# Performance work log

Measured on AMD Instinct MI355X. Metric: run time of the kernel, lower is better.

## Reference

```python
import jax, jax.numpy as jnp
import numpy as np

B, T, D, NH = 4, 2048, 768, 12
DH = D // NH
NEG = -100000.0  # module uses masked_fill with -100000.0, not -inf


def setup_inputs() -> dict:
    key = jax.random.key(0)
    ks = jax.random.split(key, 9)
    s = 1.0 / np.sqrt(D)
    return {
        "x": jax.random.normal(ks[0], (B, T, D), jnp.float32),
        "wq": jax.random.normal(ks[1], (D, D), jnp.float32) * s,
        "bq": jax.random.normal(ks[2], (D,), jnp.float32) * 0.02,
        "wk": jax.random.normal(ks[3], (D, D), jnp.float32) * s,
        "bk": jax.random.normal(ks[4], (D,), jnp.float32) * 0.02,
        "wv": jax.random.normal(ks[5], (D, D), jnp.float32) * s,
        "bv": jax.random.normal(ks[6], (D,), jnp.float32) * 0.02,
        "wo": jax.random.normal(ks[7], (D, D), jnp.float32) * s,
        "bo": jax.random.normal(ks[8], (D,), jnp.float32) * 0.02,
    }


def reference(x, wq, bq, wk, bk, wv, bv, wo, bo):
    Bx, Tx, E = x.shape
    # torch Linear: y = x @ W.T + b, weight shape [out, in]
    def heads(w, b):
        return (x @ w.T + b).reshape(Bx, Tx, NH, DH).transpose(0, 2, 1, 3)  # [B,nh,T,dh]
    Q, K, V = heads(wq, bq), heads(wk, bk), heads(wv, bv)
    scale = 1.0 / jnp.sqrt(jnp.float32(DH))
    QK = jnp.einsum("bhqd,bhkd->bhqk", Q, K) * scale  # [B,nh,T,T]
    causal = jnp.tril(jnp.ones((Tx, Tx), dtype=bool))
    QK = jnp.where(causal, QK, NEG)
    A = jax.nn.softmax(QK, axis=-1)  # attn_dropout p=0 (eval)
    Z = jnp.einsum("bhqk,bhkd->bhqd", A, V)
    Z = Z.transpose(0, 2, 1, 3).reshape(Bx, Tx, E)
    return Z @ wo.T + bo  # resid_dropout p=0 (eval)
```

## Files before the change

kernel.cpp:

```cpp
#include <hip/hip_runtime.h>


#define B_ 4
#define T_ 2048
#define D_ 768
#define NH_ 12
#define DH_ 64
#define M_ (B_ * T_)

typedef __attribute__((ext_vector_type(8))) short bf16x8;
typedef __attribute__((ext_vector_type(4))) float f32x4;
typedef __attribute__((ext_vector_type(16))) float f32x16;
typedef __attribute__((ext_vector_type(4))) unsigned int u32x4;

__device__ __forceinline__ unsigned short f2bf(float f) {
  unsigned int u = __builtin_bit_cast(unsigned int, f);
  u += 0x7FFFu + ((u >> 16) & 1u);
  return (unsigned short)(u >> 16);
}

__device__ __forceinline__ void async16(const void* g, void* l) {
  __builtin_amdgcn_global_load_lds(
      (const __attribute__((address_space(1))) unsigned int*)g,
      (__attribute__((address_space(3))) unsigned int*)l, 16, 0, 0);
}

#define RAW_BARRIER()                         \
  do {                                        \
    asm volatile("" ::: "memory");            \
    __builtin_amdgcn_s_barrier();             \
    asm volatile("" ::: "memory");            \
  } while (0)

__global__ void cvt_kernel(const float* __restrict__ x, const float* __restrict__ wq,
                           const float* __restrict__ wk, const float* __restrict__ wv,
                           const float* __restrict__ wo,
                           unsigned short* __restrict__ xb, unsigned short* __restrict__ wqb,
                           unsigned short* __restrict__ wkb, unsigned short* __restrict__ wvb,
                           unsigned short* __restrict__ wob) {
  const float* src; unsigned short* dst; int n4;
  switch (blockIdx.y) {
    case 0: src = x;  dst = xb;  n4 = M_ * D_ / 4; break;
    case 1: src = wq; dst = wqb; n4 = D_ * D_ / 4; break;
    case 2: src = wk; dst = wkb; n4 = D_ * D_ / 4; break;
    case 3: src = wv; dst = wvb; n4 = D_ * D_ / 4; break;
    default: src = wo; dst = wob; n4 = D_ * D_ / 4; break;
  }
  int stride = gridDim.x * blockDim.x;
  for (int i = blockIdx.x * blockDim.x + threadIdx.x; i < n4; i += stride) {
    float4 v = ((const float4*)src)[i];
    ushort4 o;
    o.x = f2bf(v.x); o.y = f2bf(v.y); o.z = f2bf(v.z); o.w = f2bf(v.w);
    ((ushort4*)dst)[i] = o;
  }
}

__global__ __launch_bounds__(512, 4) void gemm_kernel(
    const unsigned short* __restrict__ A,
    const unsigned short* __restrict__ W0, const unsigned short* __restrict__ W1,
    const unsigned short* __restrict__ W2,
    const float* __restrict__ bias0, const float* __restrict__ bias1,
    const float* __restrict__ bias2,
    void* out0, void* out1, void* out2,
    float s0, int K, int qkv) {
  __shared__ __align__(16) char lds[73728];

  int bid = blockIdx.x;
  int xcd = bid & 7, g = bid >> 3;
  int mt, nt;
  if (qkv) { mt = xcd + (g / 9) * 8; nt = g % 9; }
  else     { mt = xcd + (g / 3) * 8;  nt = g % 3; }
  int y  = qkv ? nt / 3 : 0;
  int nW = qkv ? nt % 3 : nt;
  const unsigned short* W = y == 0 ? W0 : (y == 1 ? W1 : W2);
  const float* bias = y == 0 ? bias0 : (y == 1 ? bias1 : bias2);
  void* outp = y == 0 ? out0 : (y == 1 ? out1 : out2);
  float scl = (qkv && y == 0) ? s0 : 1.0f;
  int mode = qkv ? ((y == 2) ? 2 : 1) : 0;

  int tid = threadIdx.x, lane = tid & 63, wid = tid >> 6;
  int l15 = lane & 15, l4 = lane >> 4;
  int wm = wid >> 2, wn = wid & 3;
  int m0 = mt << 7, n0w = nW << 8;

  int aRow, aCol;
  {
    int row = wid * 16 + (lane >> 2);
    int colE = (lane & 3) * 8;
    aRow = row;
    aCol = colE ^ (((row >> 1) & 3) << 3);
  }
  int bRow[2], bCol[2];
#pragma unroll
  for (int c = 0; c < 2; ++c) {
    int u = c * 8 + wid;
    int row = u * 16 + (lane >> 2);
    int colE = (lane & 3) * 8;
    bRow[c] = row;
    bCol[c] = colE ^ (((row >> 1) & 3) << 3);
  }

  int aoff[4], boff[4];
#pragma unroll
  for (int mf = 0; mf < 4; ++mf) {
    int row = wm * 64 + mf * 16 + l15;
    aoff[mf] = row * 64 + ((l4 * 16) ^ (((row >> 1) & 3) << 4));
  }
#pragma unroll
  for (int nf = 0; nf < 4; ++nf) {
    int row = wn * 64 + nf * 16 + l15;
    boff[nf] = 8192 + row * 64 + ((l4 * 16) ^ (((row >> 1) & 3) << 4));
  }

  const unsigned short* Wb = W + (size_t)n0w * K;

#define ISSUE_TILE(kt, slot)                                                       \
  do {                                                                             \
    async16(A + (size_t)(m0 + aRow) * K + (kt) + aCol, (slot) + wid * 1024);       \
    _Pragma("unroll") for (int c = 0; c < 2; ++c)                                  \
      async16(Wb + (size_t)bRow[c] * K + (kt) + bCol[c],                           \
              (slot) + 8192 + (c * 8 + wid) * 1024);                               \
  } while (0)

  f32x4 acc[4][4] = {};
  char* b0 = lds;
  char* b1 = lds + 24576;
  char* b2 = lds + 49152;

  ISSUE_TILE(0, b0);
  ISSUE_TILE(32, b1);

  int NT = K >> 5;
#pragma unroll 1
  for (int t = 0; t < NT; ++t) {
    if (t + 1 < NT) asm volatile("s_waitcnt vmcnt(3)" ::: "memory");
    else            asm volatile("s_waitcnt vmcnt(0)" ::: "memory");
    RAW_BARRIER();
    if (t + 2 < NT) ISSUE_TILE((t + 2) << 5, b2);
    bf16x8 af[4], bfr[4];
#pragma unroll
    for (int mf = 0; mf < 4; ++mf) af[mf] = *(const bf16x8*)(b0 + aoff[mf]);
#pragma unroll
    for (int nf = 0; nf < 4; ++nf) bfr[nf] = *(const bf16x8*)(b0 + boff[nf]);
    __builtin_amdgcn_s_setprio(1);
#pragma unroll
    for (int mf = 0; mf < 4; ++mf)
#pragma unroll
      for (int nf = 0; nf < 4; ++nf)
        acc[mf][nf] = __builtin_amdgcn_mfma_f32_16x16x32_bf16(af[mf], bfr[nf], acc[mf][nf], 0, 0, 0);
    __builtin_amdgcn_s_setprio(0);
    char* tmp = b0; b0 = b1; b1 = b2; b2 = tmp;
  }
#undef ISSUE_TILE

  if (mode == 2) {
#pragma unroll
    for (int nf = 0; nf < 4; ++nf) {
      int colW = n0w + wn * 64 + nf * 16 + l15;
      float bv = bias[colW];
      int h = colW >> 6, d = colW & 63;
#pragma unroll
      for (int mf = 0; mf < 4; ++mf) {
        int rbase = m0 + wm * 64 + mf * 16 + l4 * 4;
        int bb = rbase >> 11, tt = rbase & (T_ - 1);
        ushort4 o;
        o.x = f2bf(acc[mf][nf][0] + bv);
        o.y = f2bf(acc[mf][nf][1] + bv);
        o.z = f2bf(acc[mf][nf][2] + bv);
        o.w = f2bf(acc[mf][nf][3] + bv);
        *(ushort4*)((unsigned short*)outp + ((size_t)(bb * NH_ + h) * DH_ + d) * T_ + tt) = o;
      }
    }
  } else {
#pragma unroll
    for (int nf = 0; nf < 4; ++nf) {
      int colW = n0w + wn * 64 + nf * 16 + l15;
      float bv = bias[colW];
#pragma unroll
      for (int mf = 0; mf < 4; ++mf) {
        int rbase = m0 + wm * 64 + mf * 16 + l4 * 4;
#pragma unroll
        for (int r = 0; r < 4; ++r) {
          float v = (acc[mf][nf][r] + bv) * scl;
          size_t idx = (size_t)(rbase + r) * D_ + colW;
          if (mode == 1) ((unsigned short*)outp)[idx] = f2bf(v);
          else           ((float*)outp)[idx] = v;
        }
      }
    }
  }
}

__global__ __launch_bounds__(256, 2) void attn_kernel(
    const unsigned short* __restrict__ Q, const unsigned short* __restrict__ Kg,
    const unsigned short* __restrict__ VT, unsigned short* __restrict__ Z) {
  __shared__ __align__(16) char lds[65536];

  int tid = threadIdx.x, lane = tid & 63, w = tid >> 6;
  int l31 = lane & 31, hi = lane >> 5;
  int bid = blockIdx.x;
  int xcd = bid & 7, g = bid >> 3;
  int qt = 15 - g / 6;
  int bh = xcd + (g % 6) * 8;
  int b = bh / NH_, h = bh % NH_;
  int q0 = qt * 128;
  int qrow = q0 + w * 32 + l31;

  const unsigned short* Qb = Q + (size_t)(b * T_) * D_ + h * DH_;
  const unsigned short* Kb = Kg + (size_t)(b * T_) * D_ + h * DH_;
  const unsigned short* VTb = VT + (size_t)(b * NH_ + h) * DH_ * T_;

  bf16x8 qf[4];
#pragma unroll
  for (int s = 0; s < 4; ++s)
    qf[s] = *(const bf16x8*)(Qb + (size_t)qrow * D_ + s * 16 + hi * 8);

  int sRow[2], sCol[2];
#pragma unroll
  for (int c = 0; c < 2; ++c) {
    int pos = ((c * 4 + w) * 64 + lane) * 8;
    int row = pos >> 6, colE = pos & 63;
    sRow[c] = row;
    sCol[c] = colE ^ ((row & 7) << 3);
  }

  int koff[2][4];
#pragma unroll
  for (int n = 0; n < 2; ++n)
#pragma unroll
    for (int s = 0; s < 4; ++s) {
      int row = n * 32 + l31;
      koff[n][s] = row * 128 + ((s * 32 + hi * 16) ^ ((row & 7) << 4));
    }

  f32x16 zt[2] = {};
  float l_run = 0.f;
  int ntiles = 2 * qt + 2;

#define STAGE(tt)                                                                  \
  do {                                                                             \
    int kv0 = (tt) * 64;                                                           \
    int kb = ((tt) & 3) << 13;                                                     \
    _Pragma("unroll") for (int c = 0; c < 2; ++c) {                                \
      async16(Kb + (size_t)(kv0 + sRow[c]) * D_ + sCol[c],                         \
              lds + kb + (c * 4 + w) * 1024);                                      \
      async16(VTb + (size_t)sRow[c] * T_ + kv0 + sCol[c],                          \
              lds + 32768 + kb + (c * 4 + w) * 1024);                              \
    }                                                                              \
  } while (0)

  STAGE(0);
  STAGE(1);

#pragma unroll 1
  for (int t = 0; t < ntiles; ++t) {
    if ((t & 1) == 0) {
      __syncthreads();
      if (t + 2 < ntiles) {
        STAGE(t + 2);
        STAGE(t + 3);
      }
    }
    const char* kbase = lds + ((t & 3) << 13);
    const char* vbase = lds + 32768 + ((t & 3) << 13);

    f32x16 st[2];
    __builtin_amdgcn_s_setprio(1);
#pragma unroll
    for (int n = 0; n < 2; ++n) {
      f32x16 a = {};
#pragma unroll
      for (int s = 0; s < 4; ++s) {
        bf16x8 kf = *(const bf16x8*)(kbase + koff[n][s]);
        a = __builtin_amdgcn_mfma_f32_32x32x16_bf16(kf, qf[s], a, 0, 0, 0);
      }
      st[n] = a;
    }
    __builtin_amdgcn_s_setprio(0);

    if (t >= 2 * qt) {
      int kvb = t * 64;
#pragma unroll
      for (int n = 0; n < 2; ++n)
#pragma unroll
        for (int m = 0; m < 4; ++m)
#pragma unroll
          for (int c2 = 0; c2 < 4; ++c2) {
            int kv = kvb + n * 32 + m * 8 + hi * 4 + c2;
            if (kv > qrow) st[n][m * 4 + c2] = -1e30f;
          }
    }

    bf16x8 pb[4];
#pragma unroll
    for (int n = 0; n < 2; ++n) {
      float u[16];
#pragma unroll
      for (int r = 0; r < 16; ++r) {
        u[r] = __builtin_amdgcn_exp2f(st[n][r]);
        l_run += u[r];
      }
#pragma unroll
      for (int hf = 0; hf < 2; ++hf) {
        unsigned int A0, A1, B0, B1;
        asm("v_cvt_pk_bf16_f32 %0, %1, %2" : "=v"(A0) : "v"(u[hf*8+0]), "v"(u[hf*8+1]));
        asm("v_cvt_pk_bf16_f32 %0, %1, %2" : "=v"(A1) : "v"(u[hf*8+2]), "v"(u[hf*8+3]));
        asm("v_cvt_pk_bf16_f32 %0, %1, %2" : "=v"(B0) : "v"(u[hf*8+4]), "v"(u[hf*8+5]));
        asm("v_cvt_pk_bf16_f32 %0, %1, %2" : "=v"(B1) : "v"(u[hf*8+6]), "v"(u[hf*8+7]));
        asm("v_permlane32_swap_b32 %0, %1" : "+v"(A0), "+v"(B0));
        asm("v_permlane32_swap_b32 %0, %1" : "+v"(A1), "+v"(B1));
        u32x4 pk; pk[0] = A0; pk[1] = A1; pk[2] = B0; pk[3] = B1;
        pb[n * 2 + hf] = __builtin_bit_cast(bf16x8, pk);
      }
    }

    __builtin_amdgcn_s_setprio(1);
#pragma unroll
    for (int dt = 0; dt < 2; ++dt) {
#pragma unroll
      for (int s = 0; s < 4; ++s) {
        bf16x8 vf = *(const bf16x8*)(vbase + koff[dt][s]);
        zt[dt] = __builtin_amdgcn_mfma_f32_32x32x16_bf16(vf, pb[s], zt[dt], 0, 0, 0);
      }
    }
    __builtin_amdgcn_s_setprio(0);
  }
#undef STAGE

  l_run += __shfl_xor(l_run, 32);
  float inv = __builtin_amdgcn_rcpf(l_run);
  unsigned short* Zrow = Z + (size_t)(b * T_ + qrow) * D_ + h * DH_;
#pragma unroll
  for (int dt = 0; dt < 2; ++dt)
#pragma unroll
    for (int m = 0; m < 4; ++m) {
      ushort4 o;
      o.x = f2bf(zt[dt][m * 4 + 0] * inv);
      o.y = f2bf(zt[dt][m * 4 + 1] * inv);
      o.z = f2bf(zt[dt][m * 4 + 2] * inv);
      o.w = f2bf(zt[dt][m * 4 + 3] * inv);
      *(ushort4*)(Zrow + dt * 32 + m * 8 + hi * 4) = o;
    }
}

extern "C" void kernel_launch(void* const* d_in, const int* in_sizes, int n_in,
                              void* d_out, int out_size, void* d_ws, size_t ws_size,
                              hipStream_t stream) {
  (void)in_sizes; (void)n_in; (void)out_size; (void)ws_size;
  const float* x  = (const float*)d_in[0];
  const float* wq = (const float*)d_in[1];
  const float* bq = (const float*)d_in[2];
  const float* wk = (const float*)d_in[3];
  const float* bk = (const float*)d_in[4];
  const float* wv = (const float*)d_in[5];
  const float* bv = (const float*)d_in[6];
  const float* wo = (const float*)d_in[7];
  const float* bo = (const float*)d_in[8];

  char* ws = (char*)d_ws;
  const size_t XB = (size_t)M_ * D_ * 2;
  const size_t WB = (size_t)D_ * D_ * 2;
  unsigned short* xb  = (unsigned short*)(ws);
  unsigned short* wqb = (unsigned short*)(ws + XB);
  unsigned short* wkb = (unsigned short*)(ws + XB + WB);
  unsigned short* wvb = (unsigned short*)(ws + XB + 2 * WB);
  unsigned short* wob = (unsigned short*)(ws + XB + 3 * WB);
  unsigned short* Qb  = (unsigned short*)(ws + XB + 4 * WB);
  unsigned short* Kb  = (unsigned short*)(ws + XB + 4 * WB + XB);
  unsigned short* VTb = (unsigned short*)(ws + XB + 4 * WB + 2 * XB);
  unsigned short* Zb  = xb;

  const float SCALE_Q = 0.125f * 1.44269504f;

  cvt_kernel<<<dim3(1024, 5), 256, 0, stream>>>(x, wq, wk, wv, wo, xb, wqb, wkb, wvb, wob);
  gemm_kernel<<<dim3(576), 512, 0, stream>>>(
      xb, wqb, wkb, wvb, bq, bk, bv, Qb, Kb, VTb, SCALE_Q, D_, 1);
  attn_kernel<<<dim3(768), 256, 0, stream>>>(Qb, Kb, VTb, Zb);
  gemm_kernel<<<dim3(192), 512, 0, stream>>>(
      Zb, wob, wob, wob, bo, bo, bo, d_out, d_out, d_out, 1.0f, D_, 0);
}
```

Before: 115.0 us.

## Process two query row-blocks per attention workgroup to reuse K/V tiles

Each attention workgroup now handles 256 query rows, as two 128-row halves per wave, instead of 128. Every K/V tile staged in LDS feeds MFMAs for both halves, and the first half skips the last tiles that lie beyond its causal limit. This halves K/V global-to-LDS traffic and the grid size (768 to 384 blocks), at the cost of doubled accumulator and Q-fragment registers, possible lower occupancy, and fewer blocks to balance causal work across CUs.

After: 131.1 us. +14.0%, slower.

```diff
diff --git a/kernel.cpp b/kernel.cpp
--- a/kernel.cpp
+++ b/kernel.cpp
@@ -200,20 +200,23 @@
   int l31 = lane & 31, hi = lane >> 5;
   int bid = blockIdx.x;
   int xcd = bid & 7, g = bid >> 3;
-  int qt = 15 - g / 6;
+  int qt = 7 - g / 6;
   int bh = xcd + (g % 6) * 8;
   int b = bh / NH_, h = bh % NH_;
-  int q0 = qt * 128;
-  int qrow = q0 + w * 32 + l31;
+  int q0 = qt * 256;
+  int qrow1 = q0 + w * 32 + l31;
+  int qrow2 = qrow1 + 128;
 
   const unsigned short* Qb = Q + (size_t)(b * T_) * D_ + h * DH_;
   const unsigned short* Kb = Kg + (size_t)(b * T_) * D_ + h * DH_;
   const unsigned short* VTb = VT + (size_t)(b * NH_ + h) * DH_ * T_;
 
-  bf16x8 qf[4];
-#pragma unroll
-  for (int s = 0; s < 4; ++s)
-    qf[s] = *(const bf16x8*)(Qb + (size_t)qrow * D_ + s * 16 + hi * 8);
+  bf16x8 qf1[4], qf2[4];
+#pragma unroll
+  for (int s = 0; s < 4; ++s) {
+    qf1[s] = *(const bf16x8*)(Qb + (size_t)qrow1 * D_ + s * 16 + hi * 8);
+    qf2[s] = *(const bf16x8*)(Qb + (size_t)qrow2 * D_ + s * 16 + hi * 8);
+  }
 
   int sRow[2], sCol[2];
 #pragma unroll
@@ -233,9 +236,10 @@
       koff[n][s] = row * 128 + ((s * 32 + hi * 16) ^ ((row & 7) << 4));
     }
 
-  f32x16 zt[2] = {};
-  float l_run = 0.f;
-  int ntiles = 2 * qt + 2;
+  f32x16 zt1[2] = {}, zt2[2] = {};
+  float l1 = 0.f, l2 = 0.f;
+  int ntiles = 4 * qt + 4;
+  int h1lim = 4 * qt + 2;
 
 #define STAGE(tt)                                                                  \
   do {                                                                             \
@@ -249,6 +253,33 @@
     }                                                                              \
   } while (0)
 
+#define SMAX(a, pb, lr, MASKED, kvb_, n_, qrow_)                                   \
+  do {                                                                             \
+    if (MASKED) {                                                                  \
+      _Pragma("unroll") for (int m = 0; m < 4; ++m)                                \
+        _Pragma("unroll") for (int c2 = 0; c2 < 4; ++c2) {                         \
+          int kv = (kvb_) + (n_) * 32 + m * 8 + hi * 4 + c2;                       \
+          if (kv > (qrow_)) (a)[m * 4 + c2] = -1e30f;                              \
+        }                                                                          \
+    }                                                                              \
+    float u[16];                                                                   \
+    _Pragma("unroll") for (int r = 0; r < 16; ++r) {                               \
+      u[r] = __builtin_amdgcn_exp2f((a)[r]);                                       \
+      (lr) += u[r];                                                                \
+    }                                                                              \
+    _Pragma("unroll") for (int hf = 0; hf < 2; ++hf) {                             \
+      unsigned int A0, A1, B0, B1;                                                 \
+      asm("v_cvt_pk_bf16_f32 %0, %1, %2" : "=v"(A0) : "v"(u[hf*8+0]), "v"(u[hf*8+1]));\
+      asm("v_cvt_pk_bf16_f32 %0, %1, %2" : "=v"(A1) : "v"(u[hf*8+2]), "v"(u[hf*8+3]));\
+      asm("v_cvt_pk_bf16_f32 %0, %1, %2" : "=v"(B0) : "v"(u[hf*8+4]), "v"(u[hf*8+5]));\
+      asm("v_cvt_pk_bf16_f32 %0, %1, %2" : "=v"(B1) : "v"(u[hf*8+6]), "v"(u[hf*8+7]));\
+      asm("v_permlane32_swap_b32 %0, %1" : "+v"(A0), "+v"(B0));                    \
+      asm("v_permlane32_swap_b32 %0, %1" : "+v"(A1), "+v"(B1));                    \
+      u32x4 pk; pk[0] = A0; pk[1] = A1; pk[2] = B0; pk[3] = B1;                    \
+      (pb)[(n_) * 2 + hf] = __builtin_bit_cast(bf16x8, pk);                        \
+    }                                                                              \
+  } while (0)
+
   STAGE(0);
   STAGE(1);
 
@@ -263,55 +294,26 @@
     }
     const char* kbase = lds + ((t & 3) << 13);
     const char* vbase = lds + 32768 + ((t & 3) << 13);
-
-    f32x16 st[2];
-    __builtin_amdgcn_s_setprio(1);
+    bool hone = (t < h1lim);
+    int kvb = t * 64;
+    bool m1 = (t >= 4 * qt);
+    bool m2 = (t >= 4 * qt + 2);
+
+    bf16x8 pb1[4], pb2[4];
 #pragma unroll
     for (int n = 0; n < 2; ++n) {
-      f32x16 a = {};
+      f32x16 a1 = {}, a2 = {};
+      __builtin_amdgcn_s_setprio(1);
 #pragma unroll
       for (int s = 0; s < 4; ++s) {
         bf16x8 kf = *(const bf16x8*)(kbase + koff[n][s]);
-        a = __builtin_amdgcn_mfma_f32_32x32x16_bf16(kf, qf[s], a, 0, 0, 0);
-      }
-      st[n] = a;
-    }
-    __builtin_amdgcn_s_setprio(0);
-
-    if (t >= 2 * qt) {
-      int kvb = t * 64;
-#pragma unroll
-      for (int n = 0; n < 2; ++n)
-#pragma unroll
-        for (int m = 0; m < 4; ++m)
-#pragma unroll
-          for (int c2 = 0; c2 < 4; ++c2) {
-            int kv = kvb + n * 32 + m * 8 + hi * 4 + c2;
-            if (kv > qrow) st[n][m * 4 + c2] = -1e30f;
-          }
-    }
-
-    bf16x8 pb[4];
-#pragma unroll
-    for (int n = 0; n < 2; ++n) {
-      float u[16];
-#pragma unroll
-      for (int r = 0; r < 16; ++r) {
-        u[r] = __builtin_amdgcn_exp2f(st[n][r]);
-        l_run += u[r];
-      }
-#pragma unroll
-      for (int hf = 0; hf < 2; ++hf) {
-        unsigned int A0, A1, B0, B1;
-        asm("v_cvt_pk_bf16_f32 %0, %1, %2" : "=v"(A0) : "v"(u[hf*8+0]), "v"(u[hf*8+1]));
-        asm("v_cvt_pk_bf16_f32 %0, %1, %2" : "=v"(A1) : "v"(u[hf*8+2]), "v"(u[hf*8+3]));
-        asm("v_cvt_pk_bf16_f32 %0, %1, %2" : "=v"(B0) : "v"(u[hf*8+4]), "v"(u[hf*8+5]));
-        asm("v_cvt_pk_bf16_f32 %0, %1, %2" : "=v"(B1) : "v"(u[hf*8+6]), "v"(u[hf*8+7]));
-        asm("v_permlane32_swap_b32 %0, %1" : "+v"(A0), "+v"(B0));
-        asm("v_permlane32_swap_b32 %0, %1" : "+v"(A1), "+v"(B1));
-        u32x4 pk; pk[0] = A0; pk[1] = A1; pk[2] = B0; pk[3] = B1;
-        pb[n * 2 + hf] = __builtin_bit_cast(bf16x8, pk);
-      }
+        a2 = __builtin_amdgcn_mfma_f32_32x32x16_bf16(kf, qf2[s], a2, 0, 0, 0);
+        if (hone)
+          a1 = __builtin_amdgcn_mfma_f32_32x32x16_bf16(kf, qf1[s], a1, 0, 0, 0);
+      }
+      __builtin_amdgcn_s_setprio(0);
+      SMAX(a2, pb2, l2, m2, kvb, n, qrow2);
+      if (hone) SMAX(a1, pb1, l1, m1, kvb, n, qrow1);
     }
 
     __builtin_amdgcn_s_setprio(1);
@@ -320,26 +322,37 @@
 #pragma unroll
       for (int s = 0; s < 4; ++s) {
         bf16x8 vf = *(const bf16x8*)(vbase + koff[dt][s]);
-        zt[dt] = __builtin_amdgcn_mfma_f32_32x32x16_bf16(vf, pb[s], zt[dt], 0, 0, 0);
+        zt2[dt] = __builtin_amdgcn_mfma_f32_32x32x16_bf16(vf, pb2[s], zt2[dt], 0, 0, 0);
+        if (hone)
+          zt1[dt] = __builtin_amdgcn_mfma_f32_32x32x16_bf16(vf, pb1[s], zt1[dt], 0, 0, 0);
       }
     }
     __builtin_amdgcn_s_setprio(0);
   }
 #undef STAGE
-
-  l_run += __shfl_xor(l_run, 32);
-  float inv = __builtin_amdgcn_rcpf(l_run);
-  unsigned short* Zrow = Z + (size_t)(b * T_ + qrow) * D_ + h * DH_;
+#undef SMAX
+
+  l1 += __shfl_xor(l1, 32);
+  l2 += __shfl_xor(l2, 32);
+  float inv1 = __builtin_amdgcn_rcpf(l1);
+  float inv2 = __builtin_amdgcn_rcpf(l2);
+  unsigned short* Zrow1 = Z + (size_t)(b * T_ + qrow1) * D_ + h * DH_;
+  unsigned short* Zrow2 = Z + (size_t)(b * T_ + qrow2) * D_ + h * DH_;
 #pragma unroll
   for (int dt = 0; dt < 2; ++dt)
 #pragma unroll
     for (int m = 0; m < 4; ++m) {
-      ushort4 o;
-      o.x = f2bf(zt[dt][m * 4 + 0] * inv);
-      o.y = f2bf(zt[dt][m * 4 + 1] * inv);
-      o.z = f2bf(zt[dt][m * 4 + 2] * inv);
-      o.w = f2bf(zt[dt][m * 4 + 3] * inv);
-      *(ushort4*)(Zrow + dt * 32 + m * 8 + hi * 4) = o;
+      ushort4 o1, o2;
+      o1.x = f2bf(zt1[dt][m * 4 + 0] * inv1);
+      o1.y = f2bf(zt1[dt][m * 4 + 1] * inv1);
+      o1.z = f2bf(zt1[dt][m * 4 + 2] * inv1);
+      o1.w = f2bf(zt1[dt][m * 4 + 3] * inv1);
+      *(ushort4*)(Zrow1 + dt * 32 + m * 8 + hi * 4) = o1;
+      o2.x = f2bf(zt2[dt][m * 4 + 0] * inv2);
+      o2.y = f2bf(zt2[dt][m * 4 + 1] * inv2);
+      o2.z = f2bf(zt2[dt][m * 4 + 2] * inv2);
+      o2.w = f2bf(zt2[dt][m * 4 + 3] * inv2);
+      *(ushort4*)(Zrow2 + dt * 32 + m * 8 + hi * 4) = o2;
     }
 }
 
@@ -375,7 +388,7 @@
   cvt_kernel<<<dim3(1024, 5), 256, 0, stream>>>(x, wq, wk, wv, wo, xb, wqb, wkb, wvb, wob);
   gemm_kernel<<<dim3(576), 512, 0, stream>>>(
       xb, wqb, wkb, wvb, bq, bk, bv, Qb, Kb, VTb, SCALE_Q, D_, 1);
-  attn_kernel<<<dim3(768), 256, 0, stream>>>(Qb, Kb, VTb, Zb);
+  attn_kernel<<<dim3(384), 256, 0, stream>>>(Qb, Kb, VTb, Zb);
   gemm_kernel<<<dim3(192), 512, 0, stream>>>(
       Zb, wob, wob, wob, bo, bo, bo, d_out, d_out, d_out, 1.0f, D_, 0);
 }
```
